# Performance work log

Measured on AMD Instinct MI355X. Metric: run time of the kernel, lower is better.

Reference implementation:

```python
import jax, jax.numpy as jnp
import numpy as np

B, T = 512, 64
A, H, R = 6, 256, 256
SS, SD = 32, 32          # stochastic_size, stochastic_dim
L = SS * SD              # latent_dim = 1024


def setup_inputs() -> dict:
    key = jax.random.key(0)
    ks = jax.random.split(key, 12)
    s = 0.05
    obs = jax.random.normal(ks[0], (B, T, H), dtype=jnp.float32)
    action = jax.random.normal(ks[1], (B, T, A), dtype=jnp.float32)
    first = jax.random.bernoulli(ks[2], 0.1, (B, T, 1))
    u = jax.random.uniform(ks[3], (T, B, SS, SD), minval=1e-6, maxval=1.0 - 1e-6)
    gumbel = -jnp.log(-jnp.log(u))  # Gumbel(0,1) noise for categorical sampling
    W_in = jax.random.normal(ks[4], (H, L + A)) * s
    b_in = jax.random.normal(ks[5], (H,)) * s
    W_ih = jax.random.normal(ks[6], (3 * R, H)) * s
    W_hh = jax.random.normal(ks[7], (3 * R, R)) * s
    b_ih = jax.random.normal(ks[8], (3 * R,)) * s
    b_hh = jax.random.normal(ks[9], (3 * R,)) * s
    W_post = jax.random.normal(ks[10], (L, R + H)) * s
    b_post = jax.random.normal(ks[11], (L,)) * s
    return {"obs": obs, "action": action, "first": first, "gumbel": gumbel,
            "W_in": W_in, "b_in": b_in, "W_ih": W_ih, "W_hh": W_hh,
            "b_ih": b_ih, "b_hh": b_hh, "W_post": W_post, "b_post": b_post}


def reference(obs, action, first, gumbel, W_in, b_in, W_ih, W_hh, b_ih, b_hh, W_post, b_post):
    bs = obs.shape[0]
    rec = W_hh.shape[1]
    latent = W_post.shape[0]
    size, dim = gumbel.shape[-2], gumbel.shape[-1]

    def step(carry, xs):
        deter, stoch = carry
        o, a, f, g = xs  # per-timestep slices
        # reset to initial (zeros) where episode starts
        deter = jnp.where(f, 0.0, deter)
        stoch = jnp.where(f, 0.0, stoch)
        # img_step: in-linear + GRUCell (torch gate order r, z, n)
        x = jnp.concatenate([stoch, a], axis=-1) @ W_in.T + b_in
        gi = x @ W_ih.T + b_ih
        gh = deter @ W_hh.T + b_hh
        i_r, i_z, i_n = jnp.split(gi, 3, axis=-1)
        h_r, h_z, h_n = jnp.split(gh, 3, axis=-1)
        r = jax.nn.sigmoid(i_r + h_r)
        z = jax.nn.sigmoid(i_z + h_z)
        n = jnp.tanh(i_n + r * h_n)
        h = (1.0 - z) * n + z * deter  # new deter
        # posterior head + categorical sample (Gumbel-max, non-differentiable)
        logits = jnp.concatenate([h, o], axis=-1) @ W_post.T + b_post
        lg = logits.reshape(bs, size, dim)
        idx = jnp.argmax(lg + g, axis=-1)
        stoch_new = jax.nn.one_hot(idx, dim, dtype=logits.dtype).reshape(bs, latent)
        return (h, stoch_new), (h, stoch_new, logits)

    carry0 = (jnp.zeros((bs, rec), obs.dtype), jnp.zeros((bs, latent), obs.dtype))
    xs = (jnp.swapaxes(obs, 0, 1), jnp.swapaxes(action, 0, 1),
          jnp.swapaxes(first, 0, 1), gumbel)
    _, (deter_seq, stoch_seq, logits_seq) = jax.lax.scan(step, carry0, xs)
    # back to batch-first [B, T, ...]
    return (jnp.swapaxes(deter_seq, 0, 1),
            jnp.swapaxes(stoch_seq, 0, 1),
            jnp.swapaxes(logits_seq, 0, 1))
```

## Files before the change

kernel.cpp:

```cpp
#include <hip/hip_runtime.h>
#include <math.h>

#define BB   512
#define TT   64
#define AD   6
#define HD   256
#define RD   256
#define LD   1024
#define GD   768

#define OFF_WIHT    0u
#define OFF_WHHT    196608u
#define OFF_WPOSTT  393216u
#define OFF_WCT     917504u
#define OFF_BC      1708544u
#define OFF_OBSPROJ 1709312u
#define WS_FLOATS_FULL (OFF_OBSPROJ + (size_t)32768 * 1024)

__device__ __forceinline__ void fma4(float4& a, const float4 w, const float s) {
  a.x = fmaf(w.x, s, a.x); a.y = fmaf(w.y, s, a.y);
  a.z = fmaf(w.z, s, a.z); a.w = fmaf(w.w, s, a.w);
}
__device__ __forceinline__ void fma2(float2& a, const float2 w, const float s) {
  a.x = fmaf(w.x, s, a.x); a.y = fmaf(w.y, s, a.y);
}
typedef float fvec4 __attribute__((ext_vector_type(4)));
__device__ __forceinline__ float4 ntload4(const float* p) {
  const fvec4 v = __builtin_nontemporal_load((const fvec4*)p);
  return make_float4(v.x, v.y, v.z, v.w);
}
__device__ __forceinline__ void ntstore4(float* p, const float4 v) {
  fvec4 w; w.x = v.x; w.y = v.y; w.z = v.z; w.w = v.w;
  __builtin_nontemporal_store(w, (fvec4*)p);
}

__global__ __launch_bounds__(256) void transpose_k(const float* __restrict__ src,
                                                   float* __restrict__ dst,
                                                   int R, int C) {
  __shared__ float t_s[32][33];
  const int tx = threadIdx.x, ty = threadIdx.y;
  const int c0 = blockIdx.x * 32, r0 = blockIdx.y * 32;
#pragma unroll
  for (int k = 0; k < 4; ++k)
    t_s[ty + k*8][tx] = src[(size_t)(r0 + ty + k*8) * C + c0 + tx];
  __syncthreads();
#pragma unroll
  for (int k = 0; k < 4; ++k)
    dst[(size_t)(c0 + ty + k*8) * R + r0 + tx] = t_s[tx][ty + k*8];
}

__global__ __launch_bounds__(256) void wc_kernel(const float* __restrict__ W_in,
                                                 const float* __restrict__ b_in,
                                                 const float* __restrict__ WihT,
                                                 const float* __restrict__ b_ih,
                                                 float* __restrict__ WcT,
                                                 float* __restrict__ bc) {
  __shared__ float v_s[256];
  const int tid = threadIdx.x;
  const int col = blockIdx.x;
  v_s[tid] = (col < 1030) ? W_in[(size_t)tid * 1030 + col] : b_in[tid];
  __syncthreads();
  float a0 = 0.f, a1 = 0.f, a2 = 0.f;
#pragma unroll 4
  for (int h = 0; h < 256; ++h) {
    const float v = v_s[h];
    const float* row = &WihT[(size_t)h * GD];
    a0 = fmaf(row[tid      ], v, a0);
    a1 = fmaf(row[tid + 256], v, a1);
    a2 = fmaf(row[tid + 512], v, a2);
  }
  if (col < 1030) {
    WcT[(size_t)col * GD + tid      ] = a0;
    WcT[(size_t)col * GD + tid + 256] = a1;
    WcT[(size_t)col * GD + tid + 512] = a2;
  } else {
    bc[tid      ] = b_ih[tid      ] + a0;
    bc[tid + 256] = b_ih[tid + 256] + a1;
    bc[tid + 512] = b_ih[tid + 512] + a2;
  }
}

__global__ __launch_bounds__(256) void obsproj_gemm(const float* __restrict__ obs,
                                                    const float* __restrict__ Wpost,
                                                    const float* __restrict__ bpost,
                                                    float* __restrict__ outp) {
  __shared__ __align__(16) float As[32][132];
  __shared__ __align__(16) float Bs[32][132];
  const int tid = threadIdx.x;
  const int tx = tid & 15, ty = tid >> 4;
  const int m0 = blockIdx.y * 128, n0 = blockIdx.x * 128;
  float acc[8][8];
#pragma unroll
  for (int i = 0; i < 8; ++i)
#pragma unroll
    for (int j = 0; j < 8; ++j) acc[i][j] = 0.f;

  for (int k0 = 0; k0 < 256; k0 += 32) {
#pragma unroll
    for (int it = 0; it < 4; ++it) {
      const int idx = tid + it * 256;
      const int mi = idx >> 3, k4 = (idx & 7) * 4;
      float4 va = *(const float4*)&obs[(size_t)(m0 + mi) * 256 + k0 + k4];
      As[k4+0][mi] = va.x; As[k4+1][mi] = va.y; As[k4+2][mi] = va.z; As[k4+3][mi] = va.w;
      float4 vb = *(const float4*)&Wpost[(size_t)(n0 + mi) * 512 + 256 + k0 + k4];
      Bs[k4+0][mi] = vb.x; Bs[k4+1][mi] = vb.y; Bs[k4+2][mi] = vb.z; Bs[k4+3][mi] = vb.w;
    }
    __syncthreads();
#pragma unroll 8
    for (int k = 0; k < 32; ++k) {
      float4 a0 = *(const float4*)&As[k][ty*4];
      float4 a1 = *(const float4*)&As[k][64 + ty*4];
      float4 b0 = *(const float4*)&Bs[k][tx*4];
      float4 b1 = *(const float4*)&Bs[k][64 + tx*4];
      float av[8] = {a0.x,a0.y,a0.z,a0.w,a1.x,a1.y,a1.z,a1.w};
      float bv[8] = {b0.x,b0.y,b0.z,b0.w,b1.x,b1.y,b1.z,b1.w};
#pragma unroll
      for (int i = 0; i < 8; ++i)
#pragma unroll
        for (int j = 0; j < 8; ++j) acc[i][j] = fmaf(av[i], bv[j], acc[i][j]);
    }
    __syncthreads();
  }
  float4 bp0 = *(const float4*)&bpost[n0 + tx*4];
  float4 bp1 = *(const float4*)&bpost[n0 + 64 + tx*4];
#pragma unroll
  for (int i = 0; i < 8; ++i) {
    const int mi = (i < 4) ? (ty*4 + i) : (64 + ty*4 + (i - 4));
    float4 c0, c1;
    c0.x = acc[i][0] + bp0.x; c0.y = acc[i][1] + bp0.y;
    c0.z = acc[i][2] + bp0.z; c0.w = acc[i][3] + bp0.w;
    c1.x = acc[i][4] + bp1.x; c1.y = acc[i][5] + bp1.y;
    c1.z = acc[i][6] + bp1.z; c1.w = acc[i][7] + bp1.w;
    ntstore4(&outp[(size_t)(m0 + mi) * 1024 + n0 + tx*4], c0);
    ntstore4(&outp[(size_t)(m0 + mi) * 1024 + n0 + 64 + tx*4], c1);
  }
}

#define GH_LOAD(W, g) {                                                   \
    const int cg_ = (g) * 4;                                              \
    W[0] = wp[(size_t)(cg_ + 0) * 192];                                   \
    W[1] = wp[(size_t)(cg_ + 1) * 192];                                   \
    W[2] = wp[(size_t)(cg_ + 2) * 192];                                   \
    W[3] = wp[(size_t)(cg_ + 3) * 192];                                   \
  }
#define GH_LOADL(W) {                                                     \
    W[0] = ((const float4*)wpin_gh[half][0])[rg];                         \
    W[1] = ((const float4*)wpin_gh[half][1])[rg];                         \
    W[2] = ((const float4*)wpin_gh[half][2])[rg];                         \
    W[3] = ((const float4*)wpin_gh[half][3])[rg];                         \
  }
#define GH_FMA(W, g) {                                                    \
    const int cg_ = (g) * 4;                                              \
    const float4 d0 = *(const float4*)&deter_s[0][cbase + cg_];           \
    const float4 d1 = *(const float4*)&deter_s[1][cbase + cg_];           \
    const float4 d2 = *(const float4*)&deter_s[2][cbase + cg_];           \
    const float4 d3 = *(const float4*)&deter_s[3][cbase + cg_];           \
    fma4(acc0, W[0], d0.x); fma4(acc0, W[1], d0.y); fma4(acc0, W[2], d0.z); fma4(acc0, W[3], d0.w); \
    fma4(acc1, W[0], d1.x); fma4(acc1, W[1], d1.y); fma4(acc1, W[2], d1.z); fma4(acc1, W[3], d1.w); \
    fma4(acc2, W[0], d2.x); fma4(acc2, W[1], d2.y); fma4(acc2, W[2], d2.z); fma4(acc2, W[3], d2.w); \
    fma4(acc3, W[0], d3.x); fma4(acc3, W[1], d3.y); fma4(acc3, W[2], d3.z); fma4(acc3, W[3], d3.w); \
  }
#define GI_LOAD(W, g) {                                                   \
    W[0] = Wc4[(size_t)scol_s[j][(g)*4 + 0] * 192 + rg];                  \
    W[1] = Wc4[(size_t)scol_s[j][(g)*4 + 1] * 192 + rg];                  \
    W[2] = Wc4[(size_t)scol_s[j][(g)*4 + 2] * 192 + rg];                  \
    W[3] = Wc4[(size_t)scol_s[j][(g)*4 + 3] * 192 + rg];                  \
  }
#define GI_ADD(W) {                                                       \
    acc.x += W[0].x; acc.y += W[0].y; acc.z += W[0].z; acc.w += W[0].w;   \
    acc.x += W[1].x; acc.y += W[1].y; acc.z += W[1].z; acc.w += W[1].w;   \
    acc.x += W[2].x; acc.y += W[2].y; acc.z += W[2].z; acc.w += W[2].w;   \
    acc.x += W[3].x; acc.y += W[3].y; acc.z += W[3].z; acc.w += W[3].w;   \
  }
#define PP_LOAD(W, g) {                                                   \
    const int cg_ = (g) * 4;                                              \
    W[0] = pp2w[(size_t)(cg_ + 0) * 512];                                 \
    W[1] = pp2w[(size_t)(cg_ + 1) * 512];                                 \
    W[2] = pp2w[(size_t)(cg_ + 2) * 512];                                 \
    W[3] = pp2w[(size_t)(cg_ + 3) * 512];                                 \
  }
#define PP_LOADL(W, g) {                                                  \
    W[0] = ((const float2*)wpin_pp[half][g][0])[o2];                      \
    W[1] = ((const float2*)wpin_pp[half][g][1])[o2];                      \
    W[2] = ((const float2*)wpin_pp[half][g][2])[o2];                      \
    W[3] = ((const float2*)wpin_pp[half][g][3])[o2];                      \
  }
#define PP_FMA(W, g) {                                                    \
    const int cg_ = (g) * 4;                                              \
    const float4 d0 = *(const float4*)&deter_s[0][cbase + cg_];           \
    const float4 d1 = *(const float4*)&deter_s[1][cbase + cg_];           \
    const float4 d2 = *(const float4*)&deter_s[2][cbase + cg_];           \
    const float4 d3 = *(const float4*)&deter_s[3][cbase + cg_];           \
    fma2(acc0, W[0], d0.x); fma2(acc0, W[1], d0.y); fma2(acc0, W[2], d0.z); fma2(acc0, W[3], d0.w); \
    fma2(acc1, W[0], d1.x); fma2(acc1, W[1], d1.y); fma2(acc1, W[2], d1.z); fma2(acc1, W[3], d1.w); \
    fma2(acc2, W[0], d2.x); fma2(acc2, W[1], d2.y); fma2(acc2, W[2], d2.z); fma2(acc2, W[3], d2.w); \
    fma2(acc3, W[0], d3.x); fma2(acc3, W[1], d3.y); fma2(acc3, W[2], d3.z); fma2(acc3, W[3], d3.w); \
  }

__global__ __launch_bounds__(1024, 4) void rssm_scan(
    const float* __restrict__ obs, const float* __restrict__ action,
    const int* __restrict__ first, const float* __restrict__ gumbel,
    const float* __restrict__ WhhT, const float* __restrict__ WpostT,
    const float* __restrict__ WcT, const float* __restrict__ bc,
    const float* __restrict__ bhh, const float* __restrict__ bpost,
    const float* __restrict__ obsproj,
    float* __restrict__ out_deter, float* __restrict__ out_stoch,
    float* __restrict__ out_logits) {
  union SharedU {
    struct { float gi[4][GD]; float ghp[2][4][GD]; } g;
    float pp[2][4][LD];
  };
  __shared__ SharedU u;
  __shared__ __align__(16) float deter_s[4][RD];
  __shared__ __align__(16) float obs_s[4][HD];
  __shared__ float act_all[4][TT][AD];
  __shared__ int   first_all[4][TT];
  __shared__ float bc_s[GD];
  __shared__ float bhh_s[GD];
  __shared__ int   scol_s[4][32];
  __shared__ __align__(16) float wpin_gh[2][4][768];
  __shared__ __align__(16) float wpin_pp[2][2][4][1024];

  const int tid = threadIdx.x;
  const int b0 = blockIdx.x * 4;
  const bool use_op = (obsproj != nullptr);
  const float4* Wc4 = (const float4*)WcT;
  const float4* Wh4 = (const float4*)WhhT;
  const float2* Wp2 = (const float2*)WpostT;

  for (int i = tid; i < 1024; i += 1024) deter_s[i >> 8][i & 255] = 0.f;
  for (int i = tid; i < 4 * TT * AD; i += 1024) {
    const int j = i / (TT * AD), rem = i % (TT * AD);
    act_all[j][rem / AD][rem % AD] = action[(size_t)(b0 + j) * TT * AD + rem];
  }
  if (tid < 4 * TT) first_all[tid >> 6][tid & 63] = first[(b0 + (tid >> 6)) * TT + (tid & 63)];
  if (tid < GD) { bc_s[tid] = bc[tid]; bhh_s[tid] = bhh[tid]; }
  for (int i = tid; i < 1536; i += 1024) {
    const int hf = i / 768, r = i % 768, c = r / 192, rg = r % 192;
    ((float4*)wpin_gh[hf][c])[rg] = Wh4[(size_t)(hf * 128 + c) * 192 + rg];
  }
  for (int i = tid; i < 4096; i += 1024) {
    const int hf = i / 2048, r = i % 2048, g = r / 1024, r2 = r % 1024;
    const int c = r2 / 256, q = r2 % 256;
    ((float4*)wpin_pp[hf][g][c])[q] =
        ((const float4*)(WpostT + (size_t)(hf * 128 + g * 4 + c) * 1024))[q];
  }
  __syncthreads();

  const int jme = tid >> 8, o4me = tid & 255;

  for (int t = 0; t < TT; ++t) {
    float4 op4, g4;
    if (use_op)
      op4 = ntload4(&obsproj[(((size_t)(b0 + jme) * TT + t) * LD) + o4me * 4]);
    else
      op4 = *(const float4*)&bpost[o4me * 4];
    g4 = ntload4(&gumbel[(((size_t)t * BB + b0 + jme) * LD) + o4me * 4]);

    if (tid < 384) {
      const int half = (tid < 192) ? 0 : 1;
      const int rg = tid - half * 192;
      const int cbase = half * 128;
      float4 acc0, acc1, acc2, acc3;
      if (half == 0) {
        acc0 = *(const float4*)&bhh_s[rg * 4];
        acc1 = acc0; acc2 = acc0; acc3 = acc0;
      } else {
        acc0 = make_float4(0.f, 0.f, 0.f, 0.f);
        acc1 = acc0; acc2 = acc0; acc3 = acc0;
      }
      const float4* wp = &Wh4[(size_t)cbase * 192 + rg];
      float4 wA[4], wB[4], wC[4];
      GH_LOAD(wA, 1); GH_LOAD(wB, 2);
      GH_LOADL(wC); GH_FMA(wC, 0);
#pragma unroll 1
      for (int gg = 0; gg < 9; ++gg) {
        const int g = 1 + gg * 3;
        GH_LOAD(wC, g + 2); GH_FMA(wA, g);
        GH_LOAD(wA, g + 3); GH_FMA(wB, g + 1);
        GH_LOAD(wB, g + 4); GH_FMA(wC, g + 2);
      }
      GH_LOAD(wC, 30); GH_FMA(wA, 28);
      GH_LOAD(wA, 31); GH_FMA(wB, 29);
      GH_FMA(wC, 30); GH_FMA(wA, 31);
      *(float4*)&u.g.ghp[half][0][rg * 4] = acc0;
      *(float4*)&u.g.ghp[half][1][rg * 4] = acc1;
      *(float4*)&u.g.ghp[half][2][rg * 4] = acc2;
      *(float4*)&u.g.ghp[half][3][rg * 4] = acc3;
    } else if (tid < 768) {
      const int id = tid - 384;
#pragma unroll
      for (int q = 0; q < 2; ++q) {
        const int task = id + q * 384;
        const int j = task / 192, rg = task % 192;
        float4 acc = *(const float4*)&bc_s[rg * 4];
#pragma unroll
        for (int a = 0; a < AD; ++a)
          fma4(acc, Wc4[(size_t)(LD + a) * 192 + rg], act_all[j][t][a]);
        const bool skip = (t == 0) || first_all[j][t];
        if (!skip) {
          float4 gA[4], gB[4], gC[4];
          GI_LOAD(gA, 0); GI_LOAD(gB, 1);
#pragma unroll 1
          for (int gg = 0; gg < 2; ++gg) {
            const int g = gg * 3;
            GI_LOAD(gC, g + 2); GI_ADD(gA);
            GI_LOAD(gA, g + 3); GI_ADD(gB);
            GI_LOAD(gB, g + 4); GI_ADD(gC);
          }
          GI_ADD(gA); GI_ADD(gB);
        }
        *(float4*)&u.g.gi[j][rg * 4] = acc;
      }
    } else {
      if (!use_op) {
        const int z = tid - 768;
        const int j = z >> 6, r4 = z & 63;
        *(float4*)&obs_s[j][r4 * 4] =
            ntload4(&obs[((size_t)(b0 + j) * TT + t) * HD + r4 * 4]);
      }
    }
    __syncthreads();

    {
      const int j = tid >> 8, r = tid & 255;
      const float ir = u.g.gi[j][r], iz = u.g.gi[j][r + 256], inn = u.g.gi[j][r + 512];
      const float hr = u.g.ghp[0][j][r      ] + u.g.ghp[1][j][r      ];
      const float hz = u.g.ghp[0][j][r + 256] + u.g.ghp[1][j][r + 256];
      const float hn = u.g.ghp[0][j][r + 512] + u.g.ghp[1][j][r + 512];
      const bool f = (first_all[j][t] != 0);
      const float dprev = f ? 0.f : deter_s[j][r];
      const float rr = 1.f / (1.f + __expf(-(ir + hr)));
      const float zz = 1.f / (1.f + __expf(-(iz + hz)));
      const float nn = tanhf(fmaf(rr, hn, inn));
      const float h = (1.f - zz) * nn + zz * dprev;
      deter_s[j][r] = h;
      __builtin_nontemporal_store(h, &out_deter[((size_t)(b0 + j) * TT + t) * RD + r]);
    }
    __syncthreads();

    {
      const int half = tid >> 9, o2 = tid & 511;
      const int cbase = half * 128;
      float2 acc0 = make_float2(0.f, 0.f), acc1 = acc0, acc2 = acc0, acc3 = acc0;
      const float2* pp2w = &Wp2[(size_t)cbase * 512 + o2];
      float2 pA[4], pB[4], pC[4];
      PP_LOAD(pA, 2); PP_LOAD(pB, 3);
      PP_LOADL(pC, 0); PP_FMA(pC, 0);
      PP_LOADL(pC, 1); PP_FMA(pC, 1);
#pragma unroll 1
      for (int gg = 0; gg < 9; ++gg) {
        const int g = 2 + gg * 3;
        PP_LOAD(pC, g + 2); PP_FMA(pA, g);
        PP_LOAD(pA, g + 3); PP_FMA(pB, g + 1);
        PP_LOAD(pB, g + 4); PP_FMA(pC, g + 2);
      }
      PP_LOAD(pC, 31); PP_FMA(pA, 29);
      PP_FMA(pB, 30); PP_FMA(pC, 31);
      if (!use_op) {
#pragma unroll 4
        for (int c = 0; c < 128; c += 4) {
          const float2 w0 = Wp2[(size_t)(256 + cbase + c + 0) * 512 + o2];
          const float2 w1 = Wp2[(size_t)(256 + cbase + c + 1) * 512 + o2];
          const float2 w2 = Wp2[(size_t)(256 + cbase + c + 2) * 512 + o2];
          const float2 w3 = Wp2[(size_t)(256 + cbase + c + 3) * 512 + o2];
          const float4 o0 = *(const float4*)&obs_s[0][cbase + c];
          const float4 o1 = *(const float4*)&obs_s[1][cbase + c];
          const float4 o2v = *(const float4*)&obs_s[2][cbase + c];
          const float4 o3 = *(const float4*)&obs_s[3][cbase + c];
          fma2(acc0, w0, o0.x); fma2(acc0, w1, o0.y); fma2(acc0, w2, o0.z); fma2(acc0, w3, o0.w);
          fma2(acc1, w0, o1.x); fma2(acc1, w1, o1.y); fma2(acc1, w2, o1.z); fma2(acc1, w3, o1.w);
          fma2(acc2, w0, o2v.x); fma2(acc2, w1, o2v.y); fma2(acc2, w2, o2v.z); fma2(acc2, w3, o2v.w);
          fma2(acc3, w0, o3.x); fma2(acc3, w1, o3.y); fma2(acc3, w2, o3.z); fma2(acc3, w3, o3.w);
        }
      }
      *(float2*)&u.pp[half][0][o2 * 2] = acc0;
      *(float2*)&u.pp[half][1][o2 * 2] = acc1;
      *(float2*)&u.pp[half][2][o2 * 2] = acc2;
      *(float2*)&u.pp[half][3][o2 * 2] = acc3;
    }
    __syncthreads();

    {
      const float4 p0 = *(const float4*)&u.pp[0][jme][o4me * 4];
      const float4 p1 = *(const float4*)&u.pp[1][jme][o4me * 4];
      float4 l;
      l.x = p0.x + p1.x + op4.x; l.y = p0.y + p1.y + op4.y;
      l.z = p0.z + p1.z + op4.z; l.w = p0.w + p1.w + op4.w;
      ntstore4(&out_logits[((size_t)(b0 + jme) * TT + t) * LD + o4me * 4], l);
      float v[4] = {l.x + g4.x, l.y + g4.y, l.z + g4.z, l.w + g4.w};
      const int l0 = o4me * 4;
      float mv = v[0]; int mi = l0;
#pragma unroll
      for (int i = 1; i < 4; ++i)
        if (v[i] > mv) { mv = v[i]; mi = l0 + i; }
#pragma unroll
      for (int off = 1; off < 8; off <<= 1) {
        const float ov = __shfl_xor(mv, off);
        const int   oi = __shfl_xor(mi, off);
        if (ov > mv || (ov == mv && oi < mi)) { mv = ov; mi = oi; }
      }
      if ((o4me & 7) == 0) scol_s[jme][o4me >> 3] = mi;
      float4 oh;
      oh.x = (mi == l0 + 0) ? 1.f : 0.f;
      oh.y = (mi == l0 + 1) ? 1.f : 0.f;
      oh.z = (mi == l0 + 2) ? 1.f : 0.f;
      oh.w = (mi == l0 + 3) ? 1.f : 0.f;
      ntstore4(&out_stoch[((size_t)(b0 + jme) * TT + t) * LD + l0], oh);
      if (tid < 256) {
        const int j2 = tid >> 6, r4 = tid & 63;
        if (t + 1 < TT && first_all[j2][t + 1])
          *(float4*)&deter_s[j2][r4 * 4] = make_float4(0.f, 0.f, 0.f, 0.f);
      }
    }
    __syncthreads();
  }
}

extern "C" void kernel_launch(void* const* d_in, const int* in_sizes, int n_in,
                              void* d_out, int out_size, void* d_ws, size_t ws_size,
                              hipStream_t stream) {
  const float* obs    = (const float*)d_in[0];
  const float* action = (const float*)d_in[1];
  const int*   first  = (const int*)d_in[2];
  const float* gumbel = (const float*)d_in[3];
  const float* W_in   = (const float*)d_in[4];
  const float* b_in   = (const float*)d_in[5];
  const float* W_ih   = (const float*)d_in[6];
  const float* W_hh   = (const float*)d_in[7];
  const float* b_ih   = (const float*)d_in[8];
  const float* b_hh   = (const float*)d_in[9];
  const float* W_post = (const float*)d_in[10];
  const float* b_post = (const float*)d_in[11];

  float* ws      = (float*)d_ws;
  float* WihT    = ws + OFF_WIHT;
  float* WhhT    = ws + OFF_WHHT;
  float* WpostT  = ws + OFF_WPOSTT;
  float* WcT     = ws + OFF_WCT;
  float* bc      = ws + OFF_BC;
  float* obsproj = ws + OFF_OBSPROJ;
  const bool use_op = ws_size >= WS_FLOATS_FULL * sizeof(float);

  float* out_deter  = (float*)d_out;
  float* out_stoch  = out_deter + (size_t)BB * TT * RD;
  float* out_logits = out_stoch + (size_t)BB * TT * LD;

  transpose_k<<<dim3(256/32, 768/32), dim3(32, 8), 0, stream>>>(W_ih, WihT, 768, 256);
  transpose_k<<<dim3(256/32, 768/32), dim3(32, 8), 0, stream>>>(W_hh, WhhT, 768, 256);
  transpose_k<<<dim3(512/32, 1024/32), dim3(32, 8), 0, stream>>>(W_post, WpostT, 1024, 512);
  wc_kernel<<<1031, 256, 0, stream>>>(W_in, b_in, WihT, b_ih, WcT, bc);
  if (use_op)
    obsproj_gemm<<<dim3(1024/128, 32768/128), 256, 0, stream>>>(obs, W_post, b_post, obsproj);
  rssm_scan<<<128, 1024, 0, stream>>>(obs, action, first, gumbel, WhhT, WpostT, WcT, bc,
                                      b_hh, b_post, use_op ? obsproj : (const float*)nullptr,
                                      out_deter, out_stoch, out_logits);
}
```

Before: 2.832 ms.

## Halve batch rows per block to double grid size for the recurrent scan

Each block now processes 2 batch rows instead of 4, so the scan launches 256 blocks instead of 128 and can occupy more of the device's compute units. Per-thread accumulator counts, shared buffers and the gate task split are resized to match, and the gather of fused input-weight columns now uses non-temporal loads. The trade-off is less reuse of each weight load across batch rows and more total weight traffic, with many threads idle in the per-row phases.

```diff
diff --git a/kernel.cpp b/kernel.cpp
--- a/kernel.cpp
+++ b/kernel.cpp
@@ -8,6 +8,7 @@
 #define RD   256
 #define LD   1024
 #define GD   768
+#define NB   2
 
 #define OFF_WIHT    0u
 #define OFF_WHHT    196608u
@@ -153,18 +154,14 @@
     const int cg_ = (g) * 4;                                              \
     const float4 d0 = *(const float4*)&deter_s[0][cbase + cg_];           \
     const float4 d1 = *(const float4*)&deter_s[1][cbase + cg_];           \
-    const float4 d2 = *(const float4*)&deter_s[2][cbase + cg_];           \
-    const float4 d3 = *(const float4*)&deter_s[3][cbase + cg_];           \
     fma4(acc0, W[0], d0.x); fma4(acc0, W[1], d0.y); fma4(acc0, W[2], d0.z); fma4(acc0, W[3], d0.w); \
     fma4(acc1, W[0], d1.x); fma4(acc1, W[1], d1.y); fma4(acc1, W[2], d1.z); fma4(acc1, W[3], d1.w); \
-    fma4(acc2, W[0], d2.x); fma4(acc2, W[1], d2.y); fma4(acc2, W[2], d2.z); fma4(acc2, W[3], d2.w); \
-    fma4(acc3, W[0], d3.x); fma4(acc3, W[1], d3.y); fma4(acc3, W[2], d3.z); fma4(acc3, W[3], d3.w); \
   }
 #define GI_LOAD(W, g) {                                                   \
-    W[0] = Wc4[(size_t)scol_s[j][(g)*4 + 0] * 192 + rg];                  \
-    W[1] = Wc4[(size_t)scol_s[j][(g)*4 + 1] * 192 + rg];                  \
-    W[2] = Wc4[(size_t)scol_s[j][(g)*4 + 2] * 192 + rg];                  \
-    W[3] = Wc4[(size_t)scol_s[j][(g)*4 + 3] * 192 + rg];                  \
+    W[0] = ntload4((const float*)&Wc4[(size_t)scol_s[j][(g)*4 + 0] * 192 + rg]); \
+    W[1] = ntload4((const float*)&Wc4[(size_t)scol_s[j][(g)*4 + 1] * 192 + rg]); \
+    W[2] = ntload4((const float*)&Wc4[(size_t)scol_s[j][(g)*4 + 2] * 192 + rg]); \
+    W[3] = ntload4((const float*)&Wc4[(size_t)scol_s[j][(g)*4 + 3] * 192 + rg]); \
   }
 #define GI_ADD(W) {                                                       \
     acc.x += W[0].x; acc.y += W[0].y; acc.z += W[0].z; acc.w += W[0].w;   \
@@ -189,12 +186,8 @@
     const int cg_ = (g) * 4;                                              \
     const float4 d0 = *(const float4*)&deter_s[0][cbase + cg_];           \
     const float4 d1 = *(const float4*)&deter_s[1][cbase + cg_];           \
-    const float4 d2 = *(const float4*)&deter_s[2][cbase + cg_];           \
-    const float4 d3 = *(const float4*)&deter_s[3][cbase + cg_];           \
     fma2(acc0, W[0], d0.x); fma2(acc0, W[1], d0.y); fma2(acc0, W[2], d0.z); fma2(acc0, W[3], d0.w); \
     fma2(acc1, W[0], d1.x); fma2(acc1, W[1], d1.y); fma2(acc1, W[2], d1.z); fma2(acc1, W[3], d1.w); \
-    fma2(acc2, W[0], d2.x); fma2(acc2, W[1], d2.y); fma2(acc2, W[2], d2.z); fma2(acc2, W[3], d2.w); \
-    fma2(acc3, W[0], d3.x); fma2(acc3, W[1], d3.y); fma2(acc3, W[2], d3.z); fma2(acc3, W[3], d3.w); \
   }
 
 __global__ __launch_bounds__(1024, 4) void rssm_scan(
@@ -207,33 +200,33 @@
     float* __restrict__ out_deter, float* __restrict__ out_stoch,
     float* __restrict__ out_logits) {
   union SharedU {
-    struct { float gi[4][GD]; float ghp[2][4][GD]; } g;
-    float pp[2][4][LD];
+    struct { float gi[NB][GD]; float ghp[2][NB][GD]; } g;
+    float pp[2][NB][LD];
   };
   __shared__ SharedU u;
-  __shared__ __align__(16) float deter_s[4][RD];
-  __shared__ __align__(16) float obs_s[4][HD];
-  __shared__ float act_all[4][TT][AD];
-  __shared__ int   first_all[4][TT];
+  __shared__ __align__(16) float deter_s[NB][RD];
+  __shared__ __align__(16) float obs_s[NB][HD];
+  __shared__ float act_all[NB][TT][AD];
+  __shared__ int   first_all[NB][TT];
   __shared__ float bc_s[GD];
   __shared__ float bhh_s[GD];
-  __shared__ int   scol_s[4][32];
+  __shared__ int   scol_s[NB][32];
   __shared__ __align__(16) float wpin_gh[2][4][768];
   __shared__ __align__(16) float wpin_pp[2][2][4][1024];
 
   const int tid = threadIdx.x;
-  const int b0 = blockIdx.x * 4;
+  const int b0 = blockIdx.x * NB;
   const bool use_op = (obsproj != nullptr);
   const float4* Wc4 = (const float4*)WcT;
   const float4* Wh4 = (const float4*)WhhT;
   const float2* Wp2 = (const float2*)WpostT;
 
-  for (int i = tid; i < 1024; i += 1024) deter_s[i >> 8][i & 255] = 0.f;
-  for (int i = tid; i < 4 * TT * AD; i += 1024) {
-    const int j = i / (TT * AD), rem = i % (TT * AD);
+  if (tid < NB * RD) deter_s[tid >> 8][tid & 255] = 0.f;
+  if (tid < NB * TT * AD) {
+    const int j = tid / (TT * AD), rem = tid % (TT * AD);
     act_all[j][rem / AD][rem % AD] = action[(size_t)(b0 + j) * TT * AD + rem];
   }
-  if (tid < 4 * TT) first_all[tid >> 6][tid & 63] = first[(b0 + (tid >> 6)) * TT + (tid & 63)];
+  if (tid < NB * TT) first_all[tid >> 6][tid & 63] = first[(b0 + (tid >> 6)) * TT + (tid & 63)];
   if (tid < GD) { bc_s[tid] = bc[tid]; bhh_s[tid] = bhh[tid]; }
   for (int i = tid; i < 1536; i += 1024) {
     const int hf = i / 768, r = i % 768, c = r / 192, rg = r % 192;
@@ -251,23 +244,25 @@
 
   for (int t = 0; t < TT; ++t) {
     float4 op4, g4;
-    if (use_op)
-      op4 = ntload4(&obsproj[(((size_t)(b0 + jme) * TT + t) * LD) + o4me * 4]);
-    else
-      op4 = *(const float4*)&bpost[o4me * 4];
-    g4 = ntload4(&gumbel[(((size_t)t * BB + b0 + jme) * LD) + o4me * 4]);
+    if (tid < NB * 256) {
+      if (use_op)
+        op4 = ntload4(&obsproj[(((size_t)(b0 + jme) * TT + t) * LD) + o4me * 4]);
+      else
+        op4 = *(const float4*)&bpost[o4me * 4];
+      g4 = ntload4(&gumbel[(((size_t)t * BB + b0 + jme) * LD) + o4me * 4]);
+    }
 
     if (tid < 384) {
       const int half = (tid < 192) ? 0 : 1;
       const int rg = tid - half * 192;
       const int cbase = half * 128;
-      float4 acc0, acc1, acc2, acc3;
+      float4 acc0, acc1;
       if (half == 0) {
         acc0 = *(const float4*)&bhh_s[rg * 4];
-        acc1 = acc0; acc2 = acc0; acc3 = acc0;
+        acc1 = acc0;
       } else {
         acc0 = make_float4(0.f, 0.f, 0.f, 0.f);
-        acc1 = acc0; acc2 = acc0; acc3 = acc0;
+        acc1 = acc0;
       }
       const float4* wp = &Wh4[(size_t)cbase * 192 + rg];
       float4 wA[4], wB[4], wC[4];
@@ -285,44 +280,40 @@
       GH_FMA(wC, 30); GH_FMA(wA, 31);
       *(float4*)&u.g.ghp[half][0][rg * 4] = acc0;
       *(float4*)&u.g.ghp[half][1][rg * 4] = acc1;
-      *(float4*)&u.g.ghp[half][2][rg * 4] = acc2;
-      *(float4*)&u.g.ghp[half][3][rg * 4] = acc3;
     } else if (tid < 768) {
-      const int id = tid - 384;
-#pragma unroll
-      for (int q = 0; q < 2; ++q) {
-        const int task = id + q * 384;
-        const int j = task / 192, rg = task % 192;
-        float4 acc = *(const float4*)&bc_s[rg * 4];
-#pragma unroll
-        for (int a = 0; a < AD; ++a)
-          fma4(acc, Wc4[(size_t)(LD + a) * 192 + rg], act_all[j][t][a]);
-        const bool skip = (t == 0) || first_all[j][t];
-        if (!skip) {
-          float4 gA[4], gB[4], gC[4];
-          GI_LOAD(gA, 0); GI_LOAD(gB, 1);
+      const int task = tid - 384;
+      const int j = task / 192, rg = task % 192;
+      float4 acc = *(const float4*)&bc_s[rg * 4];
+#pragma unroll
+      for (int a = 0; a < AD; ++a)
+        fma4(acc, Wc4[(size_t)(LD + a) * 192 + rg], act_all[j][t][a]);
+      const bool skip = (t == 0) || first_all[j][t];
+      if (!skip) {
+        float4 gA[4], gB[4], gC[4];
+        GI_LOAD(gA, 0); GI_LOAD(gB, 1);
 #pragma unroll 1
-          for (int gg = 0; gg < 2; ++gg) {
-            const int g = gg * 3;
-            GI_LOAD(gC, g + 2); GI_ADD(gA);
-            GI_LOAD(gA, g + 3); GI_ADD(gB);
-            GI_LOAD(gB, g + 4); GI_ADD(gC);
-          }
-          GI_ADD(gA); GI_ADD(gB);
+        for (int gg = 0; gg < 2; ++gg) {
+          const int g = gg * 3;
+          GI_LOAD(gC, g + 2); GI_ADD(gA);
+          GI_LOAD(gA, g + 3); GI_ADD(gB);
+          GI_LOAD(gB, g + 4); GI_ADD(gC);
         }
-        *(float4*)&u.g.gi[j][rg * 4] = acc;
-      }
+        GI_ADD(gA); GI_ADD(gB);
+      }
+      *(float4*)&u.g.gi[j][rg * 4] = acc;
     } else {
       if (!use_op) {
         const int z = tid - 768;
-        const int j = z >> 6, r4 = z & 63;
-        *(float4*)&obs_s[j][r4 * 4] =
-            ntload4(&obs[((size_t)(b0 + j) * TT + t) * HD + r4 * 4]);
-      }
-    }
-    __syncthreads();
-
-    {
+        if (z < NB * 64) {
+          const int j = z >> 6, r4 = z & 63;
+          *(float4*)&obs_s[j][r4 * 4] =
+              ntload4(&obs[((size_t)(b0 + j) * TT + t) * HD + r4 * 4]);
+        }
+      }
+    }
+    __syncthreads();
+
+    if (tid < NB * RD) {
       const int j = tid >> 8, r = tid & 255;
       const float ir = u.g.gi[j][r], iz = u.g.gi[j][r + 256], inn = u.g.gi[j][r + 512];
       const float hr = u.g.ghp[0][j][r      ] + u.g.ghp[1][j][r      ];
@@ -342,7 +333,7 @@
     {
       const int half = tid >> 9, o2 = tid & 511;
       const int cbase = half * 128;
-      float2 acc0 = make_float2(0.f, 0.f), acc1 = acc0, acc2 = acc0, acc3 = acc0;
+      float2 acc0 = make_float2(0.f, 0.f), acc1 = acc0;
       const float2* pp2w = &Wp2[(size_t)cbase * 512 + o2];
       float2 pA[4], pB[4], pC[4];
       PP_LOAD(pA, 2); PP_LOAD(pB, 3);
@@ -366,48 +357,44 @@
           const float2 w3 = Wp2[(size_t)(256 + cbase + c + 3) * 512 + o2];
           const float4 o0 = *(const float4*)&obs_s[0][cbase + c];
           const float4 o1 = *(const float4*)&obs_s[1][cbase + c];
-          const float4 o2v = *(const float4*)&obs_s[2][cbase + c];
-          const float4 o3 = *(const float4*)&obs_s[3][cbase + c];
           fma2(acc0, w0, o0.x); fma2(acc0, w1, o0.y); fma2(acc0, w2, o0.z); fma2(acc0, w3, o0.w);
           fma2(acc1, w0, o1.x); fma2(acc1, w1, o1.y); fma2(acc1, w2, o1.z); fma2(acc1, w3, o1.w);
-          fma2(acc2, w0, o2v.x); fma2(acc2, w1, o2v.y); fma2(acc2, w2, o2v.z); fma2(acc2, w3, o2v.w);
-          fma2(acc3, w0, o3.x); fma2(acc3, w1, o3.y); fma2(acc3, w2, o3.z); fma2(acc3, w3, o3.w);
         }
       }
       *(float2*)&u.pp[half][0][o2 * 2] = acc0;
       *(float2*)&u.pp[half][1][o2 * 2] = acc1;
-      *(float2*)&u.pp[half][2][o2 * 2] = acc2;
-      *(float2*)&u.pp[half][3][o2 * 2] = acc3;
     }
     __syncthreads();
 
     {
-      const float4 p0 = *(const float4*)&u.pp[0][jme][o4me * 4];
-      const float4 p1 = *(const float4*)&u.pp[1][jme][o4me * 4];
-      float4 l;
-      l.x = p0.x + p1.x + op4.x; l.y = p0.y + p1.y + op4.y;
-      l.z = p0.z + p1.z + op4.z; l.w = p0.w + p1.w + op4.w;
-      ntstore4(&out_logits[((size_t)(b0 + jme) * TT + t) * LD + o4me * 4], l);
-      float v[4] = {l.x + g4.x, l.y + g4.y, l.z + g4.z, l.w + g4.w};
-      const int l0 = o4me * 4;
-      float mv = v[0]; int mi = l0;
-#pragma unroll
-      for (int i = 1; i < 4; ++i)
-        if (v[i] > mv) { mv = v[i]; mi = l0 + i; }
-#pragma unroll
-      for (int off = 1; off < 8; off <<= 1) {
-        const float ov = __shfl_xor(mv, off);
-        const int   oi = __shfl_xor(mi, off);
-        if (ov > mv || (ov == mv && oi < mi)) { mv = ov; mi = oi; }
-      }
-      if ((o4me & 7) == 0) scol_s[jme][o4me >> 3] = mi;
-      float4 oh;
-      oh.x = (mi == l0 + 0) ? 1.f : 0.f;
-      oh.y = (mi == l0 + 1) ? 1.f : 0.f;
-      oh.z = (mi == l0 + 2) ? 1.f : 0.f;
-      oh.w = (mi == l0 + 3) ? 1.f : 0.f;
-      ntstore4(&out_stoch[((size_t)(b0 + jme) * TT + t) * LD + l0], oh);
-      if (tid < 256) {
+      if (tid < NB * 256) {
+        const float4 p0 = *(const float4*)&u.pp[0][jme][o4me * 4];
+        const float4 p1 = *(const float4*)&u.pp[1][jme][o4me * 4];
+        float4 l;
+        l.x = p0.x + p1.x + op4.x; l.y = p0.y + p1.y + op4.y;
+        l.z = p0.z + p1.z + op4.z; l.w = p0.w + p1.w + op4.w;
+        ntstore4(&out_logits[((size_t)(b0 + jme) * TT + t) * LD + o4me * 4], l);
+        float v[4] = {l.x + g4.x, l.y + g4.y, l.z + g4.z, l.w + g4.w};
+        const int l0 = o4me * 4;
+        float mv = v[0]; int mi = l0;
+#pragma unroll
+        for (int i = 1; i < 4; ++i)
+          if (v[i] > mv) { mv = v[i]; mi = l0 + i; }
+#pragma unroll
+        for (int off = 1; off < 8; off <<= 1) {
+          const float ov = __shfl_xor(mv, off);
+          const int   oi = __shfl_xor(mi, off);
+          if (ov > mv || (ov == mv && oi < mi)) { mv = ov; mi = oi; }
+        }
+        if ((o4me & 7) == 0) scol_s[jme][o4me >> 3] = mi;
+        float4 oh;
+        oh.x = (mi == l0 + 0) ? 1.f : 0.f;
+        oh.y = (mi == l0 + 1) ? 1.f : 0.f;
+        oh.z = (mi == l0 + 2) ? 1.f : 0.f;
+        oh.w = (mi == l0 + 3) ? 1.f : 0.f;
+        ntstore4(&out_stoch[((size_t)(b0 + jme) * TT + t) * LD + l0], oh);
+      }
+      if (tid < NB * 64) {
         const int j2 = tid >> 6, r4 = tid & 63;
         if (t + 1 < TT && first_all[j2][t + 1])
           *(float4*)&deter_s[j2][r4 * 4] = make_float4(0.f, 0.f, 0.f, 0.f);
@@ -452,7 +439,7 @@
   wc_kernel<<<1031, 256, 0, stream>>>(W_in, b_in, WihT, b_ih, WcT, bc);
   if (use_op)
     obsproj_gemm<<<dim3(1024/128, 32768/128), 256, 0, stream>>>(obs, W_post, b_post, obsproj);
-  rssm_scan<<<128, 1024, 0, stream>>>(obs, action, first, gumbel, WhhT, WpostT, WcT, bc,
-                                      b_hh, b_post, use_op ? obsproj : (const float*)nullptr,
-                                      out_deter, out_stoch, out_logits);
-}
+  rssm_scan<<<BB/NB, 1024, 0, stream>>>(obs, action, first, gumbel, WhhT, WpostT, WcT, bc,
+                                        b_hh, b_post, use_op ? obsproj : (const float*)nullptr,
+                                        out_deter, out_stoch, out_logits);
+}
```

New measurement: 2.597 ms. 1.09x faster.
